# Optimization experiments

Hardware: AMD Instinct MI355X
Metric: run time of the kernel (lower is better)

Reference implementation:

```python
import jax, jax.numpy as jnp
import numpy as np

B, T, D, H = 1, 2048, 1024, 16
HD = D // H
STRIDE = T // 256  # hierarchical global stride (T > 512 branch)


def _mha(q_in, k_in, v_in, Wqkv, bqkv, Wo, bo, nh):
    """torch nn.MultiheadAttention (batch_first, eval/no-dropout), returns (out, head-avg attn)."""
    b, tq, d = q_in.shape
    hd = d // nh
    Wq, Wk, Wv = jnp.split(Wqkv, 3, axis=0)
    bq, bk, bv = jnp.split(bqkv, 3)
    def heads(x, W, bb):
        return (x @ W.T + bb).reshape(b, x.shape[1], nh, hd).transpose(0, 2, 1, 3)
    q = heads(q_in, Wq, bq)
    k = heads(k_in, Wk, bk)
    v = heads(v_in, Wv, bv)
    scores = jnp.einsum('bhtd,bhsd->bhts', q, k) / np.float32(np.sqrt(hd))
    attn = jax.nn.softmax(scores, axis=-1)
    out = jnp.einsum('bhts,bhsd->bhtd', attn, v).transpose(0, 2, 1, 3).reshape(b, tq, d)
    return out @ Wo.T + bo, attn.mean(axis=1)


def _interp_linear(x, size):
    """F.interpolate(mode='linear', align_corners=False) along axis 1. x: [B, Ts, C]."""
    ts = x.shape[1]
    src = (jnp.arange(size, dtype=x.dtype) + 0.5) * (ts / size) - 0.5
    src = jnp.clip(src, 0.0, ts - 1)
    i0 = jnp.floor(src).astype(jnp.int32)
    i1 = jnp.minimum(i0 + 1, ts - 1)
    w = (src - i0.astype(x.dtype))[None, :, None]
    return x[:, i0, :] * (1.0 - w) + x[:, i1, :] * w


def setup_inputs() -> dict:
    rng = jax.random.key(0)
    ks = iter(jax.random.split(rng, 32))
    s = 0.02
    n = lambda shape: jax.random.normal(next(ks), shape, dtype=jnp.float32) * s
    return {
        'query': jax.random.normal(next(ks), (B, T, D), jnp.float32),
        'key': jax.random.normal(next(ks), (B, T, D), jnp.float32),
        'value': jax.random.normal(next(ks), (B, T, D), jnp.float32),
        'strategy_probs': jax.nn.softmax(jax.random.normal(next(ks), (B, 4), jnp.float32), -1),
        'Wqkv_lin': n((3 * D, D)), 'b_lin': jnp.zeros((3 * D,), jnp.float32),
        'Wo_lin': n((D, D)), 'bo_lin': jnp.zeros((D,), jnp.float32),
        'sparsity_pattern': jax.random.normal(next(ks), (H, 1, 1), jnp.float32),
        'Wqkv_loc': n((3 * D, D)), 'b_loc': jnp.zeros((3 * D,), jnp.float32),
        'Wo_loc': n((D, D)), 'bo_loc': jnp.zeros((D,), jnp.float32),
        'Wqkv_glb': n((3 * D, D)), 'b_glb': jnp.zeros((3 * D,), jnp.float32),
        'Wo_glb': n((D, D)), 'bo_glb': jnp.zeros((D,), jnp.float32),
        'Wf': n((D, 2 * D)), 'bf': jnp.zeros((D,), jnp.float32),
        'R_quant': jax.random.normal(next(ks), (H, HD, HD), jnp.float32),
        'ent_gate': jax.random.normal(next(ks), (H, 2, 2), jnp.float32),
    }


def reference(query, key, value, strategy_probs, Wqkv_lin, b_lin, Wo_lin, bo_lin,
              sparsity_pattern, Wqkv_loc, b_loc, Wo_loc, bo_loc,
              Wqkv_glb, b_glb, Wo_glb, bo_glb, Wf, bf, R_quant, ent_gate):
    b, t, d = query.shape
    hd = d // H
    scale = np.float32(np.sqrt(hd))
    # --- 1) "linear" branch: standard MHA ---
    linear_out, linear_w = _mha(query, key, value, Wqkv_lin, b_lin, Wo_lin, bo_lin, H)
    # --- 2) sparse branch (per-head learned on/off mask on raw scores) ---
    qh = query.reshape(b, t, H, hd).transpose(0, 2, 1, 3)
    kh = key.reshape(b, t, H, hd).transpose(0, 2, 1, 3)
    vh = value.reshape(b, t, H, hd).transpose(0, 2, 1, 3)
    scores = jnp.einsum('bhtd,bhsd->bhts', qh, kh) / scale
    mask = (jax.nn.sigmoid(sparsity_pattern) > 0.5).astype(scores.dtype)  # [H,1,1]
    sp_attn = jax.nn.softmax(scores * mask[None], axis=-1)
    sparse_out = jnp.einsum('bhts,bhsd->bhtd', sp_attn, vh).transpose(0, 2, 1, 3).reshape(b, t, d)
    sparse_w = sp_attn.mean(axis=1)
    # --- 3) hierarchical branch (T > 512 path: strided global + linear interp) ---
    local_out, _ = _mha(query, key, value, Wqkv_loc, b_loc, Wo_loc, bo_loc, H // 2)
    gq, gk, gv = query[:, ::STRIDE], key[:, ::STRIDE], value[:, ::STRIDE]
    g_small, _ = _mha(gq, gk, gv, Wqkv_glb, b_glb, Wo_glb, bo_glb, H // 2)
    global_out = _interp_linear(g_small, t)
    hier_out = jnp.concatenate([local_out, global_out], axis=-1) @ Wf.T + bf
    # --- 4) quantum branch (per-head rotation + scalar gate on scores) ---
    q_rot = jnp.einsum('bhtd,hde->bhte', qh, R_quant)
    k_rot = jnp.einsum('bhtd,hde->bhte', kh, R_quant)
    gate = jax.nn.sigmoid(ent_gate[:, 0, 0])[None, :, None, None]  # [1,H,1,1]
    q_attn = jax.nn.softmax((jnp.einsum('bhtd,bhsd->bhts', q_rot, k_rot) / scale) * gate, axis=-1)
    quantum_out = jnp.einsum('bhts,bhsd->bhtd', q_attn, vh).transpose(0, 2, 1, 3).reshape(b, t, d)
    quantum_w = q_attn.mean(axis=1)
    # --- blend via strategy probabilities ---
    sp = strategy_probs[:, :, None]  # [B,4,1]
    all_out = jnp.stack([linear_out, sparse_out, hier_out, quantum_out], axis=1)  # [B,4,T,D]
    weighted = (all_out * sp[..., None]).sum(axis=1)  # [B,T,D]
    wstack = jnp.stack([linear_w, sparse_w, quantum_w], axis=1)  # [B,3,T,T]
    wsel = sp[:, jnp.array([0, 1, 3])][..., None, None]  # [B,3,1,1,1] (faithful to source; requires B==1)
    combined = (wstack * wsel).sum(axis=1)
    return weighted, combined
```

## Files before the change

### kernel.cpp

```cpp
#include <hip/hip_runtime.h>
#include <math.h>

#define D_MODEL 1024

typedef __attribute__((ext_vector_type(8))) short bf16x8;
typedef __attribute__((ext_vector_type(4))) float f32x4;
typedef __attribute__((ext_vector_type(8))) unsigned short u16x8;

__device__ __forceinline__ unsigned short bfr(float f) {
    unsigned u = __float_as_uint(f);
    u += 0x7fffu + ((u >> 16) & 1u);
    return (unsigned short)(u >> 16);
}
__device__ __forceinline__ float bff(unsigned short s) {
    return __uint_as_float(((unsigned)s) << 16);
}
__device__ __forceinline__ void split2(float x, unsigned short &h, unsigned short &l) {
    h = bfr(x);
    l = bfr(x - bff(h));
}
__device__ __forceinline__ f32x4 mfma3(bf16x8 ah, bf16x8 al, bf16x8 bh, bf16x8 bl, f32x4 c) {
    c = __builtin_amdgcn_mfma_f32_16x16x32_bf16(ah, bh, c, 0, 0, 0);
    c = __builtin_amdgcn_mfma_f32_16x16x32_bf16(ah, bl, c, 0, 0, 0);
    c = __builtin_amdgcn_mfma_f32_16x16x32_bf16(al, bh, c, 0, 0, 0);
    return c;
}

__global__ __launch_bounds__(256) void split_rm(
    const float* __restrict__ in, unsigned short* __restrict__ hi,
    unsigned short* __restrict__ lo, int n4)
{
    int idx = blockIdx.x * 256 + threadIdx.x;
    if (idx >= n4) return;
    float4 v = ((const float4*)in)[idx];
    ushort4 hs, ls;
    split2(v.x, hs.x, ls.x); split2(v.y, hs.y, ls.y);
    split2(v.z, hs.z, ls.z); split2(v.w, hs.w, ls.w);
    ((ushort4*)hi)[idx] = hs;
    ((ushort4*)lo)[idx] = ls;
}

__global__ __launch_bounds__(256) void split_tr(
    const float* __restrict__ in, unsigned short* __restrict__ hi,
    unsigned short* __restrict__ lo, int T)
{
    __shared__ float xs[64][65];
    const int t0 = blockIdx.x * 64, d0 = blockIdx.y * 64;
    for (int idx = threadIdx.x; idx < 64 * 16; idx += 256) {
        int r = idx >> 4, c4 = (idx & 15) * 4;
        float4 v = *(const float4*)&in[(size_t)(t0 + r) * D_MODEL + d0 + c4];
        xs[r][c4] = v.x; xs[r][c4 + 1] = v.y; xs[r][c4 + 2] = v.z; xs[r][c4 + 3] = v.w;
    }
    __syncthreads();
    for (int idx = threadIdx.x; idx < 64 * 8; idx += 256) {
        int dd = idx >> 3, t8 = (idx & 7) * 8;
        u16x8 hs, ls;
#pragma unroll
        for (int j = 0; j < 8; ++j) {
            unsigned short hh, ll;
            split2(xs[t8 + j][dd], hh, ll);
            hs[j] = hh; ls[j] = ll;
        }
        *(u16x8*)&hi[(size_t)(d0 + dd) * T + t0 + t8] = hs;
        *(u16x8*)&lo[(size_t)(d0 + dd) * T + t0 + t8] = ls;
    }
}

__global__ __launch_bounds__(256) void gemm_mfma(
    const float* __restrict__ X, int xrstride,
    const float* __restrict__ W, int wrstride,
    const float* __restrict__ bias,
    float* __restrict__ C, int M, int N, int K,
    const float* __restrict__ sptr, int sidx, int accum)
{
    __shared__ unsigned short Xh[64][40], Xl[64][40];
    __shared__ unsigned short Wh[64][40], Wl[64][40];
    const int tid = threadIdx.x;
    const int m0 = blockIdx.x * 64, n0 = blockIdx.y * 64;
    const int lane = tid & 63, wave = tid >> 6;
    const int c = lane & 15, quad = lane >> 4;
    const int mbase = wave * 16;

    f32x4 acc[4];
#pragma unroll
    for (int nt = 0; nt < 4; ++nt) acc[nt] = (f32x4){0.f, 0.f, 0.f, 0.f};

    float4 xr[2], wr[2];
    const int r_ = tid >> 3, d4_ = (tid & 7) * 4;
    const int r2_ = (tid + 256) >> 3, d42_ = ((tid + 256) & 7) * 4;
    auto ldXW = [&](int k0) {
        xr[0] = *(const float4*)&X[(size_t)(m0 + r_) * xrstride + k0 + d4_];
        xr[1] = *(const float4*)&X[(size_t)(m0 + r2_) * xrstride + k0 + d42_];
        wr[0] = *(const float4*)&W[(size_t)(n0 + r_) * wrstride + k0 + d4_];
        wr[1] = *(const float4*)&W[(size_t)(n0 + r2_) * wrstride + k0 + d42_];
    };
    ldXW(0);

    for (int k0 = 0; k0 < K; k0 += 32) {
        __syncthreads();
        {
            ushort4 hs, ls;
            split2(xr[0].x, hs.x, ls.x); split2(xr[0].y, hs.y, ls.y);
            split2(xr[0].z, hs.z, ls.z); split2(xr[0].w, hs.w, ls.w);
            *(ushort4*)&Xh[r_][d4_] = hs; *(ushort4*)&Xl[r_][d4_] = ls;
            split2(xr[1].x, hs.x, ls.x); split2(xr[1].y, hs.y, ls.y);
            split2(xr[1].z, hs.z, ls.z); split2(xr[1].w, hs.w, ls.w);
            *(ushort4*)&Xh[r2_][d42_] = hs; *(ushort4*)&Xl[r2_][d42_] = ls;
            split2(wr[0].x, hs.x, ls.x); split2(wr[0].y, hs.y, ls.y);
            split2(wr[0].z, hs.z, ls.z); split2(wr[0].w, hs.w, ls.w);
            *(ushort4*)&Wh[r_][d4_] = hs; *(ushort4*)&Wl[r_][d4_] = ls;
            split2(wr[1].x, hs.x, ls.x); split2(wr[1].y, hs.y, ls.y);
            split2(wr[1].z, hs.z, ls.z); split2(wr[1].w, hs.w, ls.w);
            *(ushort4*)&Wh[r2_][d42_] = hs; *(ushort4*)&Wl[r2_][d42_] = ls;
        }
        __syncthreads();
        if (k0 + 32 < K) ldXW(k0 + 32);
        bf16x8 ah = *(const bf16x8*)&Xh[mbase + c][quad * 8];
        bf16x8 al = *(const bf16x8*)&Xl[mbase + c][quad * 8];
#pragma unroll
        for (int nt = 0; nt < 4; ++nt) {
            bf16x8 bh = *(const bf16x8*)&Wh[nt * 16 + c][quad * 8];
            bf16x8 bl = *(const bf16x8*)&Wl[nt * 16 + c][quad * 8];
            acc[nt] = mfma3(ah, al, bh, bl, acc[nt]);
        }
    }
    const float s = (sptr != nullptr) ? sptr[sidx] : 1.0f;
#pragma unroll
    for (int nt = 0; nt < 4; ++nt) {
#pragma unroll
        for (int reg = 0; reg < 4; ++reg) {
            int row = m0 + mbase + quad * 4 + reg;
            int col = n0 + nt * 16 + c;
            float v = acc[nt][reg] + (bias ? bias[col] : 0.0f);
            v *= s;
            size_t gi = (size_t)row * N + col;
            if (accum) v += C[gi];
            C[gi] = v;
        }
    }
}

template <int HD>
__global__ __launch_bounds__(256) void flash_mfma(
    const float* __restrict__ Q,
    const unsigned short* __restrict__ Khi, const unsigned short* __restrict__ Klo,
    const unsigned short* __restrict__ Vthi, const unsigned short* __restrict__ Vtlo,
    const float* __restrict__ aparam, int amode,
    float* __restrict__ O, float* __restrict__ O2,
    const float* __restrict__ strat, int o_sidx, int accum,
    float* __restrict__ mout, float* __restrict__ lout,
    int Tq, int Tk, float inv_scale)
{
    constexpr int ROWS = 64;
    constexpr int STILE = (HD == 64) ? 64 : 32;
    constexpr int NT_S = STILE / 16;
    constexpr int KS   = HD / 32;
    constexpr int NT_O = HD / 16;
    constexpr int KS_PV = STILE / 32;
    constexpr int QP = HD + 8;
    constexpr int SP = STILE + 8;
    constexpr int KIT = STILE * HD / 8 / 256;
    constexpr int VIT = STILE * HD / 8 / 256;

    __shared__ __align__(16) unsigned short Kh[STILE][QP], Kl[STILE][QP];
    __shared__ __align__(16) unsigned short Vh[HD][SP],  Vl[HD][SP];
    __shared__ __align__(16) unsigned short Ph[ROWS][SP], Pl[ROWS][SP];

    const int tid = threadIdx.x;
    const int h = blockIdx.y;
    const int r0 = blockIdx.x * ROWS;
    const int lane = tid & 63, wave = tid >> 6;
    const int c = lane & 15, quad = lane >> 4;
    const int mbase = wave * 16;
    const int ZS = gridDim.z;
    const int tkloc = Tk / ZS;
    const int kv0 = blockIdx.z * tkloc;

    float gate = 1.0f;
    if (amode == 1) gate = (aparam[h] > 0.0f) ? 1.0f : 0.0f;
    if (amode == 2) gate = 1.0f / (1.0f + __expf(-aparam[h * 4]));
    const float ascale = gate * inv_scale;
    const bool masked = (amode == 1) && (gate == 0.0f);

    if (masked) {
        for (int idx = tid; idx < ROWS * STILE; idx += 256) {
            int r = idx / STILE, cc = idx % STILE;
            Ph[r][cc] = 0x3F80; Pl[r][cc] = 0;
        }
    }

    bf16x8 qah[KS], qal[KS];
    if (!masked) {
        const float* qrow = &Q[(size_t)(r0 + mbase + c) * D_MODEL + h * HD];
#pragma unroll
        for (int ks = 0; ks < KS; ++ks) {
            float4 a  = *(const float4*)(qrow + ks * 32 + quad * 8);
            float4 b2 = *(const float4*)(qrow + ks * 32 + quad * 8 + 4);
            unsigned short hh, ll;
            split2(a.x, hh, ll);  qah[ks][0] = (short)hh; qal[ks][0] = (short)ll;
            split2(a.y, hh, ll);  qah[ks][1] = (short)hh; qal[ks][1] = (short)ll;
            split2(a.z, hh, ll);  qah[ks][2] = (short)hh; qal[ks][2] = (short)ll;
            split2(a.w, hh, ll);  qah[ks][3] = (short)hh; qal[ks][3] = (short)ll;
            split2(b2.x, hh, ll); qah[ks][4] = (short)hh; qal[ks][4] = (short)ll;
            split2(b2.y, hh, ll); qah[ks][5] = (short)hh; qal[ks][5] = (short)ll;
            split2(b2.z, hh, ll); qah[ks][6] = (short)hh; qal[ks][6] = (short)ll;
            split2(b2.w, hh, ll); qah[ks][7] = (short)hh; qal[ks][7] = (short)ll;
        }
    }

    float mreg[4], lacc[4];
#pragma unroll
    for (int i = 0; i < 4; ++i) { mreg[i] = -1e30f; lacc[i] = 0.0f; }
    f32x4 oacc[NT_O];
#pragma unroll
    for (int nt = 0; nt < NT_O; ++nt) oacc[nt] = (f32x4){0.f, 0.f, 0.f, 0.f};

    u16x8 krh[KIT], krl[KIT], vrh[VIT], vrl[VIT];

    auto load_regs = [&](int s0) {
        if (!masked) {
#pragma unroll
            for (int it = 0; it < KIT; ++it) {
                int idx = tid + it * 256;
                int r = idx / (HD / 8), c8 = (idx % (HD / 8)) * 8;
                size_t go = (size_t)(s0 + r) * D_MODEL + h * HD + c8;
                krh[it] = *(const u16x8*)&Khi[go];
                krl[it] = *(const u16x8*)&Klo[go];
            }
        }
#pragma unroll
        for (int it = 0; it < VIT; ++it) {
            int idx = tid + it * 256;
            int d = idx % HD, s8 = (idx / HD) * 8;
            size_t go = (size_t)(h * HD + d) * Tk + s0 + s8;
            vrh[it] = *(const u16x8*)&Vthi[go];
            vrl[it] = *(const u16x8*)&Vtlo[go];
        }
    };
    auto write_bufs = [&]() {
        if (!masked) {
#pragma unroll
            for (int it = 0; it < KIT; ++it) {
                int idx = tid + it * 256;
                int r = idx / (HD / 8), c8 = (idx % (HD / 8)) * 8;
                *(u16x8*)&Kh[r][c8] = krh[it];
                *(u16x8*)&Kl[r][c8] = krl[it];
            }
        }
#pragma unroll
        for (int it = 0; it < VIT; ++it) {
            int idx = tid + it * 256;
            int d = idx % HD, s8 = (idx / HD) * 8;
            *(u16x8*)&Vh[d][s8] = vrh[it];
            *(u16x8*)&Vl[d][s8] = vrl[it];
        }
    };

    auto compute_tile = [&]() {
        if (!masked) {
            f32x4 sf[NT_S];
#pragma unroll
            for (int nt = 0; nt < NT_S; ++nt) {
                f32x4 s = (f32x4){0.f, 0.f, 0.f, 0.f};
#pragma unroll
                for (int ks = 0; ks < KS; ++ks) {
                    bf16x8 bh = *(const bf16x8*)&Kh[nt * 16 + c][ks * 32 + quad * 8];
                    bf16x8 bl = *(const bf16x8*)&Kl[nt * 16 + c][ks * 32 + quad * 8];
                    s = mfma3(qah[ks], qal[ks], bh, bl, s);
                }
                sf[nt] = s * ascale;
            }
            float tm[4];
#pragma unroll
            for (int reg = 0; reg < 4; ++reg) tm[reg] = sf[0][reg];
#pragma unroll
            for (int nt = 1; nt < NT_S; ++nt)
#pragma unroll
                for (int reg = 0; reg < 4; ++reg) tm[reg] = fmaxf(tm[reg], sf[nt][reg]);
            bool need = (tm[0] > mreg[0] + 8.0f) || (tm[1] > mreg[1] + 8.0f) ||
                        (tm[2] > mreg[2] + 8.0f) || (tm[3] > mreg[3] + 8.0f);
            if (__any(need)) {
#pragma unroll
                for (int off = 1; off < 16; off <<= 1)
#pragma unroll
                    for (int reg = 0; reg < 4; ++reg)
                        tm[reg] = fmaxf(tm[reg], __shfl_xor(tm[reg], off));
#pragma unroll
                for (int reg = 0; reg < 4; ++reg) {
                    float nm = fmaxf(mreg[reg], tm[reg]);
                    float al = __expf(mreg[reg] - nm);
                    mreg[reg] = nm;
                    lacc[reg] *= al;
#pragma unroll
                    for (int nt = 0; nt < NT_O; ++nt) oacc[nt][reg] *= al;
                }
            }
#pragma unroll
            for (int nt = 0; nt < NT_S; ++nt) {
#pragma unroll
                for (int reg = 0; reg < 4; ++reg) {
                    float p = __expf(sf[nt][reg] - mreg[reg]);
                    lacc[reg] += p;
                    unsigned short hh, ll;
                    split2(p, hh, ll);
                    int row = mbase + quad * 4 + reg;
                    Ph[row][nt * 16 + c] = hh;
                    Pl[row][nt * 16 + c] = ll;
                }
            }
        }
        bf16x8 pah[KS_PV], pal[KS_PV];
#pragma unroll
        for (int ks = 0; ks < KS_PV; ++ks) {
            pah[ks] = *(const bf16x8*)&Ph[mbase + c][ks * 32 + quad * 8];
            pal[ks] = *(const bf16x8*)&Pl[mbase + c][ks * 32 + quad * 8];
        }
#pragma unroll
        for (int nt = 0; nt < NT_O; ++nt) {
            f32x4 o = oacc[nt];
#pragma unroll
            for (int ks = 0; ks < KS_PV; ++ks) {
                bf16x8 bh = *(const bf16x8*)&Vh[nt * 16 + c][ks * 32 + quad * 8];
                bf16x8 bl = *(const bf16x8*)&Vl[nt * 16 + c][ks * 32 + quad * 8];
                o = mfma3(pah[ks], pal[ks], bh, bl, o);
            }
            oacc[nt] = o;
        }
    };

    const int NTL = tkloc / STILE;
    load_regs(kv0);
    for (int t = 0; t < NTL; ++t) {
        __syncthreads();
        write_bufs();
        __syncthreads();
        if (t + 1 < NTL) load_regs(kv0 + (t + 1) * STILE);
        compute_tile();
    }

#pragma unroll
    for (int off = 1; off < 16; off <<= 1)
#pragma unroll
        for (int reg = 0; reg < 4; ++reg) lacc[reg] += __shfl_xor(lacc[reg], off);

    if (ZS == 1) {
        const float osc = (o_sidx >= 0) ? strat[o_sidx] : 1.0f;
#pragma unroll
        for (int reg = 0; reg < 4; ++reg) {
            float lf = masked ? (float)Tk : lacc[reg];
            int row = r0 + mbase + quad * 4 + reg;
            if (c == 0) {
                mout[h * Tq + row] = masked ? 0.0f : mreg[reg];
                lout[h * Tq + row] = lf;
            }
            float sc = osc / lf;
#pragma unroll
            for (int nt = 0; nt < NT_O; ++nt) {
                size_t gi = (size_t)row * D_MODEL + h * HD + nt * 16 + c;
                float v = sc * oacc[nt][reg];
                if (accum) v += O[gi];
                O[gi] = v;
            }
        }
    } else {
        float* Op = (blockIdx.z == 0) ? O : O2;
#pragma unroll
        for (int reg = 0; reg < 4; ++reg) {
            float lf = masked ? (float)tkloc : lacc[reg];
            int row = r0 + mbase + quad * 4 + reg;
            if (c == 0) {
                mout[(blockIdx.z * gridDim.y + h) * Tq + row] = masked ? 0.0f : mreg[reg];
                lout[(blockIdx.z * gridDim.y + h) * Tq + row] = lf;
            }
#pragma unroll
            for (int nt = 0; nt < NT_O; ++nt)
                Op[(size_t)row * D_MODEL + h * HD + nt * 16 + c] = oacc[nt][reg];
        }
    }
}

__global__ __launch_bounds__(256) void combine2(
    const float* __restrict__ O0, const float* __restrict__ O1,
    const float* __restrict__ mp, const float* __restrict__ lp,
    float* __restrict__ O, const float* __restrict__ strat,
    int o_sidx, int accum, int Tq)
{
    const int row = blockIdx.x;
    const int c4 = threadIdx.x * 4;
    const int h = c4 >> 7;
    const float m0 = mp[h * Tq + row], m1 = mp[(8 + h) * Tq + row];
    const float l0 = lp[h * Tq + row], l1 = lp[(8 + h) * Tq + row];
    const float m = fmaxf(m0, m1);
    const float w0 = __expf(m0 - m), w1 = __expf(m1 - m);
    const float osc = (o_sidx >= 0) ? strat[o_sidx] : 1.0f;
    const float sc = osc / (l0 * w0 + l1 * w1);
    float4 a = *(const float4*)&O0[(size_t)row * D_MODEL + c4];
    float4 b = *(const float4*)&O1[(size_t)row * D_MODEL + c4];
    size_t gi = (size_t)row * D_MODEL + c4;
    float4 r;
    r.x = sc * (a.x * w0 + b.x * w1);
    r.y = sc * (a.y * w0 + b.y * w1);
    r.z = sc * (a.z * w0 + b.z * w1);
    r.w = sc * (a.w * w0 + b.w * w1);
    if (accum) {
        float4 o = *(const float4*)&O[gi];
        r.x += o.x; r.y += o.y; r.z += o.z; r.w += o.w;
    }
    *(float4*)&O[gi] = r;
}

__global__ __launch_bounds__(256) void comb_mfma(
    const float* __restrict__ Q,
    const unsigned short* __restrict__ Khi, const unsigned short* __restrict__ Klo,
    const float* __restrict__ mrow, const float* __restrict__ lrow,
    const float* __restrict__ aparam, int amode,
    const float* __restrict__ strat,
    float* __restrict__ comb, int Tq, int Tk, int nh, float inv_scale)
{
    __shared__ __align__(16) unsigned short Kh[128][72], Kl[128][72];
    const int tid = threadIdx.x;
    const int r0 = blockIdx.x * 64, c0 = blockIdx.y * 128;
    const int lane = tid & 63, wave = tid >> 6;
    const int c = lane & 15, quad = lane >> 4;
    const int mbase = wave * 16;

    f32x4 acc[8];
#pragma unroll
    for (int nt = 0; nt < 8; ++nt) acc[nt] = (f32x4){0.f, 0.f, 0.f, 0.f};

    int hlist[16]; float glist[16]; int nact = 0; float unif = 0.0f;
    for (int h = 0; h < nh; ++h) {
        float gate = 1.0f;
        if (amode == 1) gate = (aparam[h] > 0.0f) ? 1.0f : 0.0f;
        if (amode == 2) gate = 1.0f / (1.0f + __expf(-aparam[h * 4]));
        if (amode == 1 && gate == 0.0f) { unif += 1.0f; continue; }
        hlist[nact] = h; glist[nact] = gate * inv_scale; ++nact;
    }

    u16x8 krh[4], krl[4];
    auto loadK = [&](int h) {
#pragma unroll
        for (int it = 0; it < 4; ++it) {
            int idx = tid + it * 256;
            int r = idx >> 3, c8 = (idx & 7) * 8;
            size_t go = (size_t)(c0 + r) * D_MODEL + h * 64 + c8;
            krh[it] = *(const u16x8*)&Khi[go];
            krl[it] = *(const u16x8*)&Klo[go];
        }
    };
    if (nact > 0) loadK(hlist[0]);

    for (int i = 0; i < nact; ++i) {
        const int h = hlist[i];
        const float ascale = glist[i];
        __syncthreads();
#pragma unroll
        for (int it = 0; it < 4; ++it) {
            int idx = tid + it * 256;
            int r = idx >> 3, c8 = (idx & 7) * 8;
            *(u16x8*)&Kh[r][c8] = krh[it];
            *(u16x8*)&Kl[r][c8] = krl[it];
        }
        __syncthreads();
        if (i + 1 < nact) loadK(hlist[i + 1]);

        bf16x8 qah[2], qal[2];
        const float* qrow = &Q[(size_t)(r0 + mbase + c) * D_MODEL + h * 64];
#pragma unroll
        for (int ks = 0; ks < 2; ++ks) {
            float4 a  = *(const float4*)(qrow + ks * 32 + quad * 8);
            float4 b2 = *(const float4*)(qrow + ks * 32 + quad * 8 + 4);
            unsigned short hh, ll;
            split2(a.x, hh, ll);  qah[ks][0] = (short)hh; qal[ks][0] = (short)ll;
            split2(a.y, hh, ll);  qah[ks][1] = (short)hh; qal[ks][1] = (short)ll;
            split2(a.z, hh, ll);  qah[ks][2] = (short)hh; qal[ks][2] = (short)ll;
            split2(a.w, hh, ll);  qah[ks][3] = (short)hh; qal[ks][3] = (short)ll;
            split2(b2.x, hh, ll); qah[ks][4] = (short)hh; qal[ks][4] = (short)ll;
            split2(b2.y, hh, ll); qah[ks][5] = (short)hh; qal[ks][5] = (short)ll;
            split2(b2.z, hh, ll); qah[ks][6] = (short)hh; qal[ks][6] = (short)ll;
            split2(b2.w, hh, ll); qah[ks][7] = (short)hh; qal[ks][7] = (short)ll;
        }

        float mr[4], li[4];
#pragma unroll
        for (int reg = 0; reg < 4; ++reg) {
            int row = r0 + mbase + quad * 4 + reg;
            mr[reg] = mrow[h * Tq + row];
            li[reg] = 1.0f / lrow[h * Tq + row];
        }
#pragma unroll
        for (int nt = 0; nt < 8; ++nt) {
            f32x4 s = (f32x4){0.f, 0.f, 0.f, 0.f};
#pragma unroll
            for (int ks = 0; ks < 2; ++ks) {
                bf16x8 bh = *(const bf16x8*)&Kh[nt * 16 + c][ks * 32 + quad * 8];
                bf16x8 bl = *(const bf16x8*)&Kl[nt * 16 + c][ks * 32 + quad * 8];
                s = mfma3(qah[ks], qal[ks], bh, bl, s);
            }
#pragma unroll
            for (int reg = 0; reg < 4; ++reg)
                acc[nt][reg] += __expf(s[reg] * ascale - mr[reg]) * li[reg];
        }
    }
    const float csc = (strat[0] + strat[1] + strat[3]) / (float)nh;
    const float uadd = unif / (float)Tk;
#pragma unroll
    for (int nt = 0; nt < 8; ++nt) {
#pragma unroll
        for (int reg = 0; reg < 4; ++reg) {
            int row = r0 + mbase + quad * 4 + reg;
            comb[(size_t)row * Tk + c0 + nt * 16 + c] = csc * (acc[nt][reg] + uadd);
        }
    }
}

__global__ __launch_bounds__(256) void rotate_heads(
    const float* __restrict__ X, const float* __restrict__ R,
    float* __restrict__ Y)
{
    __shared__ float Rt[64][68];
    __shared__ float xs[64][68];
    const int tid = threadIdx.x;
    const int h = blockIdx.y;
    const int t0 = blockIdx.x * 64;
    for (int idx = tid; idx < 4096; idx += 256) {
        int d = idx >> 6, e = idx & 63;
        Rt[e][d] = R[h * 4096 + idx];
        xs[d][e] = X[(size_t)(t0 + d) * D_MODEL + h * 64 + e];
    }
    __syncthreads();
    const int ty = tid >> 4, tx = tid & 15;
    float acc[4][4] = {};
#pragma unroll 4
    for (int d0 = 0; d0 < 64; d0 += 4) {
        float4 rv[4];
#pragma unroll
        for (int j = 0; j < 4; ++j) rv[j] = *(const float4*)&Rt[tx * 4 + j][d0];
#pragma unroll
        for (int i = 0; i < 4; ++i) {
            float4 a = *(const float4*)&xs[ty * 4 + i][d0];
#pragma unroll
            for (int j = 0; j < 4; ++j)
                acc[i][j] += a.x * rv[j].x + a.y * rv[j].y + a.z * rv[j].z + a.w * rv[j].w;
        }
    }
#pragma unroll
    for (int i = 0; i < 4; ++i)
#pragma unroll
        for (int j = 0; j < 4; ++j)
            Y[(size_t)(t0 + ty * 4 + i) * D_MODEL + h * 64 + tx * 4 + j] = acc[i][j];
}

__global__ __launch_bounds__(256) void interp_lin(
    const float* __restrict__ G, float* __restrict__ out)
{
    const int t = blockIdx.x;
    float src = (t + 0.5f) * 0.125f - 0.5f;
    src = fminf(fmaxf(src, 0.0f), 255.0f);
    float fl = floorf(src);
    int i0 = (int)fl;
    int i1 = min(i0 + 1, 255);
    float w = src - fl;
    const float4* g0 = (const float4*)(G + (size_t)i0 * D_MODEL);
    const float4* g1 = (const float4*)(G + (size_t)i1 * D_MODEL);
    float4* o = (float4*)(out + (size_t)t * D_MODEL);
    int c = threadIdx.x;
    float4 a = g0[c], b = g1[c];
    float4 r;
    r.x = a.x * (1.0f - w) + b.x * w;
    r.y = a.y * (1.0f - w) + b.y * w;
    r.z = a.z * (1.0f - w) + b.z * w;
    r.w = a.w * (1.0f - w) + b.w * w;
    o[c] = r;
}

extern "C" void kernel_launch(void* const* d_in, const int* in_sizes, int n_in,
                              void* d_out, int out_size, void* d_ws, size_t ws_size,
                              hipStream_t stream)
{
    (void)in_sizes; (void)n_in; (void)ws_size; (void)out_size;
    const float* query    = (const float*)d_in[0];
    const float* key      = (const float*)d_in[1];
    const float* value    = (const float*)d_in[2];
    const float* strat    = (const float*)d_in[3];
    const float* Wqkv_lin = (const float*)d_in[4];
    const float* b_lin    = (const float*)d_in[5];
    const float* Wo_lin   = (const float*)d_in[6];
    const float* bo_lin   = (const float*)d_in[7];
    const float* spars    = (const float*)d_in[8];
    const float* Wqkv_loc = (const float*)d_in[9];
    const float* b_loc    = (const float*)d_in[10];
    const float* Wo_loc   = (const float*)d_in[11];
    const float* bo_loc   = (const float*)d_in[12];
    const float* Wqkv_glb = (const float*)d_in[13];
    const float* b_glb    = (const float*)d_in[14];
    const float* Wo_glb   = (const float*)d_in[15];
    const float* bo_glb   = (const float*)d_in[16];
    const float* Wf       = (const float*)d_in[17];
    const float* bf       = (const float*)d_in[18];
    const float* Rq       = (const float*)d_in[19];
    const float* ent      = (const float*)d_in[20];

    float* out = (float*)d_out;
    float* weighted = out;
    float* combined = out + (size_t)2048 * 1024;
    const size_t PLANE = (size_t)2048 * 2048;

    float* ws   = (float*)d_ws;
    float* qkv  = ws;
    float* AO   = qkv + 6291456;
    float* LO   = AO + 2097152;
    float* gqkv = LO + 2097152;
    float* gAO  = gqkv + 786432;
    float* gOUT = gAO + 262144;
    float* GI   = gOUT + 262144;
    float* mb   = GI + 2097152;
    float* lb   = mb + 32768;
    float* qrot = qkv;
    float* krot = qkv + 2097152;
    unsigned short* Ksp_h = (unsigned short*)(lb + 32768);
    unsigned short* Ksp_l = Ksp_h + 2097152;
    unsigned short* Vtp_h = Ksp_l + 2097152;
    unsigned short* Vtp_l = Vtp_h + 2097152;
    unsigned short* gKs_h = Vtp_l + 2097152;
    unsigned short* gKs_l = gKs_h + 262144;
    unsigned short* gVt_h = gKs_l + 262144;
    unsigned short* gVt_l = gVt_h + 262144;

    const float inv8   = 0.125f;
    const float inv128 = 1.0f / sqrtf(128.0f);
    const float* srcs[3] = {query, key, value};

    hipMemsetAsync(weighted, 0, (size_t)2097152 * sizeof(float), stream);

    for (int sl = 0; sl < 3; ++sl)
        gemm_mfma<<<dim3(32, 16), 256, 0, stream>>>(
            srcs[sl], 1024, Wqkv_lin + (size_t)sl * 1048576, 1024, b_lin + sl * 1024,
            qkv + (size_t)sl * 2097152, 2048, 1024, 1024, nullptr, 0, 0);
    split_rm<<<dim3(2048), 256, 0, stream>>>(qkv + 2097152, Ksp_h, Ksp_l, 524288);
    split_tr<<<dim3(32, 16), 256, 0, stream>>>(qkv + 4194304, Vtp_h, Vtp_l, 2048);
    flash_mfma<64><<<dim3(32, 16), 256, 0, stream>>>(
        qkv, Ksp_h, Ksp_l, Vtp_h, Vtp_l, nullptr, 0,
        AO, nullptr, strat, -1, 0, mb, lb, 2048, 2048, inv8);
    comb_mfma<<<dim3(32, 16), 256, 0, stream>>>(
        qkv, Ksp_h, Ksp_l, mb, lb, nullptr, 0, strat,
        combined + 0 * PLANE, 2048, 2048, 16, inv8);
    gemm_mfma<<<dim3(32, 16), 256, 0, stream>>>(
        AO, 1024, Wo_lin, 1024, bo_lin, weighted, 2048, 1024, 1024, strat, 0, 1);

    split_rm<<<dim3(2048), 256, 0, stream>>>(key, Ksp_h, Ksp_l, 524288);
    split_tr<<<dim3(32, 16), 256, 0, stream>>>(value, Vtp_h, Vtp_l, 2048);
    flash_mfma<64><<<dim3(32, 16), 256, 0, stream>>>(
        query, Ksp_h, Ksp_l, Vtp_h, Vtp_l, spars, 1,
        weighted, nullptr, strat, 1, 1, mb, lb, 2048, 2048, inv8);
    comb_mfma<<<dim3(32, 16), 256, 0, stream>>>(
        query, Ksp_h, Ksp_l, mb, lb, spars, 1, strat,
        combined + 1 * PLANE, 2048, 2048, 16, inv8);

    rotate_heads<<<dim3(32, 16), 256, 0, stream>>>(query, Rq, qrot);
    rotate_heads<<<dim3(32, 16), 256, 0, stream>>>(key, Rq, krot);
    split_rm<<<dim3(2048), 256, 0, stream>>>(krot, Ksp_h, Ksp_l, 524288);
    flash_mfma<64><<<dim3(32, 16), 256, 0, stream>>>(
        qrot, Ksp_h, Ksp_l, Vtp_h, Vtp_l, ent, 2,
        weighted, nullptr, strat, 3, 1, mb, lb, 2048, 2048, inv8);
    comb_mfma<<<dim3(32, 16), 256, 0, stream>>>(
        qrot, Ksp_h, Ksp_l, mb, lb, ent, 2, strat,
        combined + 2 * PLANE, 2048, 2048, 16, inv8);

    for (int sl = 0; sl < 3; ++sl)
        gemm_mfma<<<dim3(32, 16), 256, 0, stream>>>(
            srcs[sl], 1024, Wqkv_loc + (size_t)sl * 1048576, 1024, b_loc + sl * 1024,
            qkv + (size_t)sl * 2097152, 2048, 1024, 1024, nullptr, 0, 0);
    split_rm<<<dim3(2048), 256, 0, stream>>>(qkv + 2097152, Ksp_h, Ksp_l, 524288);
    split_tr<<<dim3(32, 16), 256, 0, stream>>>(qkv + 4194304, Vtp_h, Vtp_l, 2048);
    flash_mfma<128><<<dim3(32, 8, 2), 256, 0, stream>>>(
        qkv, Ksp_h, Ksp_l, Vtp_h, Vtp_l, nullptr, 0,
        AO, GI, strat, -1, 0, mb, lb, 2048, 2048, inv128);
    combine2<<<dim3(2048), 256, 0, stream>>>(
        AO, GI, mb, lb, AO, strat, -1, 0, 2048);
    gemm_mfma<<<dim3(32, 16), 256, 0, stream>>>(
        AO, 1024, Wo_loc, 1024, bo_loc, LO, 2048, 1024, 1024, nullptr, 0, 0);

    for (int sl = 0; sl < 3; ++sl)
        gemm_mfma<<<dim3(4, 16), 256, 0, stream>>>(
            srcs[sl], 8192, Wqkv_glb + (size_t)sl * 1048576, 1024, b_glb + sl * 1024,
            gqkv + (size_t)sl * 262144, 256, 1024, 1024, nullptr, 0, 0);
    split_rm<<<dim3(256), 256, 0, stream>>>(gqkv + 262144, gKs_h, gKs_l, 65536);
    split_tr<<<dim3(4, 16), 256, 0, stream>>>(gqkv + 524288, gVt_h, gVt_l, 256);
    flash_mfma<128><<<dim3(4, 8), 256, 0, stream>>>(
        gqkv, gKs_h, gKs_l, gVt_h, gVt_l, nullptr, 0,
        gAO, nullptr, strat, -1, 0, mb, lb, 256, 256, inv128);
    gemm_mfma<<<dim3(4, 16), 256, 0, stream>>>(
        gAO, 1024, Wo_glb, 1024, bo_glb, gOUT, 256, 1024, 1024, nullptr, 0, 0);
    interp_lin<<<dim3(2048), 256, 0, stream>>>(gOUT, GI);

    gemm_mfma<<<dim3(32, 16), 256, 0, stream>>>(
        LO, 1024, Wf, 2048, bf, weighted, 2048, 1024, 1024, strat, 2, 1);
    gemm_mfma<<<dim3(32, 16), 256, 0, stream>>>(
        GI, 1024, Wf + 1024, 2048, nullptr, weighted, 2048, 1024, 1024, strat, 2, 1);
}
```

Measured before the change: 1.291 ms.

## Transpose flash score MFMA to K·Q, pack P with cvt_pk, pre-split Q for comb

The flash kernel now computes the score tile as K×Q so that each lane owns a single query row. That reduces the row max and sum work to one scalar per lane with two cross-lane shuffles, and lets P be written to LDS as packed 64-bit stores built with v_cvt_pk_bf16_f32. The masked path feeds constant one/zero fragments directly instead of filling LDS. comb_mfma now reads Q already split into bf16 hi/lo parts, prepared by new split_rm launches into reused GI scratch, instead of splitting per block. This adds three extra kernel launches and some shuffles when rescaling.

```diff
diff --git a/kernel.cpp b/kernel.cpp
--- a/kernel.cpp
+++ b/kernel.cpp
@@ -18,6 +18,11 @@
 __device__ __forceinline__ void split2(float x, unsigned short &h, unsigned short &l) {
     h = bfr(x);
     l = bfr(x - bff(h));
+}
+__device__ __forceinline__ unsigned cvtpk(float a, float b) {
+    unsigned r;
+    asm("v_cvt_pk_bf16_f32 %0, %1, %2" : "=v"(r) : "v"(a), "v"(b));
+    return r;
 }
 __device__ __forceinline__ f32x4 mfma3(bf16x8 ah, bf16x8 al, bf16x8 bh, bf16x8 bl, f32x4 c) {
     c = __builtin_amdgcn_mfma_f32_16x16x32_bf16(ah, bh, c, 0, 0, 0);
@@ -153,7 +158,7 @@
 {
     constexpr int ROWS = 64;
     constexpr int STILE = (HD == 64) ? 64 : 32;
-    constexpr int NT_S = STILE / 16;
+    constexpr int MT   = STILE / 16;
     constexpr int KS   = HD / 32;
     constexpr int NT_O = HD / 16;
     constexpr int KS_PV = STILE / 32;
@@ -181,13 +186,6 @@
     if (amode == 2) gate = 1.0f / (1.0f + __expf(-aparam[h * 4]));
     const float ascale = gate * inv_scale;
     const bool masked = (amode == 1) && (gate == 0.0f);
-
-    if (masked) {
-        for (int idx = tid; idx < ROWS * STILE; idx += 256) {
-            int r = idx / STILE, cc = idx % STILE;
-            Ph[r][cc] = 0x3F80; Pl[r][cc] = 0;
-        }
-    }
 
     bf16x8 qah[KS], qal[KS];
     if (!masked) {
@@ -208,12 +206,14 @@
         }
     }
 
-    float mreg[4], lacc[4];
-#pragma unroll
-    for (int i = 0; i < 4; ++i) { mreg[i] = -1e30f; lacc[i] = 0.0f; }
+    float mreg = -1e30f, lacc = 0.0f;
     f32x4 oacc[NT_O];
 #pragma unroll
     for (int nt = 0; nt < NT_O; ++nt) oacc[nt] = (f32x4){0.f, 0.f, 0.f, 0.f};
+
+    bf16x8 pone, pzero;
+#pragma unroll
+    for (int j = 0; j < 8; ++j) { pone[j] = (short)0x3F80; pzero[j] = 0; }
 
     u16x8 krh[KIT], krl[KIT], vrh[VIT], vrl[VIT];
 
@@ -258,62 +258,67 @@
 
     auto compute_tile = [&]() {
         if (!masked) {
-            f32x4 sf[NT_S];
-#pragma unroll
-            for (int nt = 0; nt < NT_S; ++nt) {
+            f32x4 sf[MT];
+#pragma unroll
+            for (int mt = 0; mt < MT; ++mt) {
                 f32x4 s = (f32x4){0.f, 0.f, 0.f, 0.f};
 #pragma unroll
                 for (int ks = 0; ks < KS; ++ks) {
-                    bf16x8 bh = *(const bf16x8*)&Kh[nt * 16 + c][ks * 32 + quad * 8];
-                    bf16x8 bl = *(const bf16x8*)&Kl[nt * 16 + c][ks * 32 + quad * 8];
-                    s = mfma3(qah[ks], qal[ks], bh, bl, s);
+                    bf16x8 kh = *(const bf16x8*)&Kh[mt * 16 + c][ks * 32 + quad * 8];
+                    bf16x8 kl = *(const bf16x8*)&Kl[mt * 16 + c][ks * 32 + quad * 8];
+                    s = mfma3(kh, kl, qah[ks], qal[ks], s);
                 }
-                sf[nt] = s * ascale;
-            }
-            float tm[4];
-#pragma unroll
-            for (int reg = 0; reg < 4; ++reg) tm[reg] = sf[0][reg];
-#pragma unroll
-            for (int nt = 1; nt < NT_S; ++nt)
-#pragma unroll
-                for (int reg = 0; reg < 4; ++reg) tm[reg] = fmaxf(tm[reg], sf[nt][reg]);
-            bool need = (tm[0] > mreg[0] + 8.0f) || (tm[1] > mreg[1] + 8.0f) ||
-                        (tm[2] > mreg[2] + 8.0f) || (tm[3] > mreg[3] + 8.0f);
-            if (__any(need)) {
-#pragma unroll
-                for (int off = 1; off < 16; off <<= 1)
-#pragma unroll
-                    for (int reg = 0; reg < 4; ++reg)
-                        tm[reg] = fmaxf(tm[reg], __shfl_xor(tm[reg], off));
-#pragma unroll
-                for (int reg = 0; reg < 4; ++reg) {
-                    float nm = fmaxf(mreg[reg], tm[reg]);
-                    float al = __expf(mreg[reg] - nm);
-                    mreg[reg] = nm;
-                    lacc[reg] *= al;
-#pragma unroll
-                    for (int nt = 0; nt < NT_O; ++nt) oacc[nt][reg] *= al;
-                }
-            }
-#pragma unroll
-            for (int nt = 0; nt < NT_S; ++nt) {
-#pragma unroll
-                for (int reg = 0; reg < 4; ++reg) {
-                    float p = __expf(sf[nt][reg] - mreg[reg]);
-                    lacc[reg] += p;
-                    unsigned short hh, ll;
-                    split2(p, hh, ll);
-                    int row = mbase + quad * 4 + reg;
-                    Ph[row][nt * 16 + c] = hh;
-                    Pl[row][nt * 16 + c] = ll;
-                }
+                sf[mt] = s * ascale;
+            }
+            float tm = sf[0][0];
+#pragma unroll
+            for (int mt = 0; mt < MT; ++mt)
+#pragma unroll
+                for (int reg = 0; reg < 4; ++reg) tm = fmaxf(tm, sf[mt][reg]);
+            if (__any(tm > mreg + 8.0f)) {
+                tm = fmaxf(tm, __shfl_xor(tm, 16));
+                tm = fmaxf(tm, __shfl_xor(tm, 32));
+                float nm = fmaxf(mreg, tm);
+                float al = __expf(mreg - nm);
+                mreg = nm;
+                lacc *= al;
+                float ar[4];
+#pragma unroll
+                for (int reg = 0; reg < 4; ++reg)
+                    ar[reg] = __shfl(al, (lane & 48) | (quad * 4 + reg));
+#pragma unroll
+                for (int nt = 0; nt < NT_O; ++nt)
+#pragma unroll
+                    for (int reg = 0; reg < 4; ++reg) oacc[nt][reg] *= ar[reg];
+            }
+#pragma unroll
+            for (int mt = 0; mt < MT; ++mt) {
+                float p0 = __expf(sf[mt][0] - mreg);
+                float p1 = __expf(sf[mt][1] - mreg);
+                float p2 = __expf(sf[mt][2] - mreg);
+                float p3 = __expf(sf[mt][3] - mreg);
+                lacc += (p0 + p1) + (p2 + p3);
+                unsigned h01 = cvtpk(p0, p1), h23 = cvtpk(p2, p3);
+                float b0 = __uint_as_float(h01 << 16);
+                float b1 = __uint_as_float(h01 & 0xffff0000u);
+                float b2 = __uint_as_float(h23 << 16);
+                float b3 = __uint_as_float(h23 & 0xffff0000u);
+                unsigned l01 = cvtpk(p0 - b0, p1 - b1);
+                unsigned l23 = cvtpk(p2 - b2, p3 - b3);
+                uint2 hw; hw.x = h01; hw.y = h23;
+                uint2 lw; lw.x = l01; lw.y = l23;
+                *(uint2*)&Ph[mbase + c][mt * 16 + quad * 4] = hw;
+                *(uint2*)&Pl[mbase + c][mt * 16 + quad * 4] = lw;
             }
         }
         bf16x8 pah[KS_PV], pal[KS_PV];
 #pragma unroll
         for (int ks = 0; ks < KS_PV; ++ks) {
-            pah[ks] = *(const bf16x8*)&Ph[mbase + c][ks * 32 + quad * 8];
-            pal[ks] = *(const bf16x8*)&Pl[mbase + c][ks * 32 + quad * 8];
+            if (masked) { pah[ks] = pone; pal[ks] = pzero; }
+            else {
+                pah[ks] = *(const bf16x8*)&Ph[mbase + c][ks * 32 + quad * 8];
+                pal[ks] = *(const bf16x8*)&Pl[mbase + c][ks * 32 + quad * 8];
+            }
         }
 #pragma unroll
         for (int nt = 0; nt < NT_O; ++nt) {
@@ -338,40 +343,44 @@
         compute_tile();
     }
 
-#pragma unroll
-    for (int off = 1; off < 16; off <<= 1)
-#pragma unroll
-        for (int reg = 0; reg < 4; ++reg) lacc[reg] += __shfl_xor(lacc[reg], off);
+    lacc += __shfl_xor(lacc, 16);
+    lacc += __shfl_xor(lacc, 32);
 
     if (ZS == 1) {
         const float osc = (o_sidx >= 0) ? strat[o_sidx] : 1.0f;
+        if (quad == 0) {
+            int row = r0 + mbase + c;
+            mout[h * Tq + row] = masked ? 0.0f : mreg;
+            lout[h * Tq + row] = masked ? (float)Tk : lacc;
+        }
+        float sc[4];
 #pragma unroll
         for (int reg = 0; reg < 4; ++reg) {
-            float lf = masked ? (float)Tk : lacc[reg];
+            float lf = masked ? (float)Tk
+                              : __shfl(lacc, (lane & 48) | (quad * 4 + reg));
+            sc[reg] = osc / lf;
+        }
+#pragma unroll
+        for (int reg = 0; reg < 4; ++reg) {
             int row = r0 + mbase + quad * 4 + reg;
-            if (c == 0) {
-                mout[h * Tq + row] = masked ? 0.0f : mreg[reg];
-                lout[h * Tq + row] = lf;
-            }
-            float sc = osc / lf;
 #pragma unroll
             for (int nt = 0; nt < NT_O; ++nt) {
                 size_t gi = (size_t)row * D_MODEL + h * HD + nt * 16 + c;
-                float v = sc * oacc[nt][reg];
+                float v = sc[reg] * oacc[nt][reg];
                 if (accum) v += O[gi];
                 O[gi] = v;
             }
         }
     } else {
         float* Op = (blockIdx.z == 0) ? O : O2;
+        if (quad == 0) {
+            int row = r0 + mbase + c;
+            mout[(blockIdx.z * gridDim.y + h) * Tq + row] = masked ? 0.0f : mreg;
+            lout[(blockIdx.z * gridDim.y + h) * Tq + row] = masked ? (float)tkloc : lacc;
+        }
 #pragma unroll
         for (int reg = 0; reg < 4; ++reg) {
-            float lf = masked ? (float)tkloc : lacc[reg];
             int row = r0 + mbase + quad * 4 + reg;
-            if (c == 0) {
-                mout[(blockIdx.z * gridDim.y + h) * Tq + row] = masked ? 0.0f : mreg[reg];
-                lout[(blockIdx.z * gridDim.y + h) * Tq + row] = lf;
-            }
 #pragma unroll
             for (int nt = 0; nt < NT_O; ++nt)
                 Op[(size_t)row * D_MODEL + h * HD + nt * 16 + c] = oacc[nt][reg];
@@ -410,7 +419,7 @@
 }
 
 __global__ __launch_bounds__(256) void comb_mfma(
-    const float* __restrict__ Q,
+    const unsigned short* __restrict__ Qhi, const unsigned short* __restrict__ Qlo,
     const unsigned short* __restrict__ Khi, const unsigned short* __restrict__ Klo,
     const float* __restrict__ mrow, const float* __restrict__ lrow,
     const float* __restrict__ aparam, int amode,
@@ -465,20 +474,12 @@
         if (i + 1 < nact) loadK(hlist[i + 1]);
 
         bf16x8 qah[2], qal[2];
-        const float* qrow = &Q[(size_t)(r0 + mbase + c) * D_MODEL + h * 64];
+        const unsigned short* qh = &Qhi[(size_t)(r0 + mbase + c) * D_MODEL + h * 64];
+        const unsigned short* ql = &Qlo[(size_t)(r0 + mbase + c) * D_MODEL + h * 64];
 #pragma unroll
         for (int ks = 0; ks < 2; ++ks) {
-            float4 a  = *(const float4*)(qrow + ks * 32 + quad * 8);
-            float4 b2 = *(const float4*)(qrow + ks * 32 + quad * 8 + 4);
-            unsigned short hh, ll;
-            split2(a.x, hh, ll);  qah[ks][0] = (short)hh; qal[ks][0] = (short)ll;
-            split2(a.y, hh, ll);  qah[ks][1] = (short)hh; qal[ks][1] = (short)ll;
-            split2(a.z, hh, ll);  qah[ks][2] = (short)hh; qal[ks][2] = (short)ll;
-            split2(a.w, hh, ll);  qah[ks][3] = (short)hh; qal[ks][3] = (short)ll;
-            split2(b2.x, hh, ll); qah[ks][4] = (short)hh; qal[ks][4] = (short)ll;
-            split2(b2.y, hh, ll); qah[ks][5] = (short)hh; qal[ks][5] = (short)ll;
-            split2(b2.z, hh, ll); qah[ks][6] = (short)hh; qal[ks][6] = (short)ll;
-            split2(b2.w, hh, ll); qah[ks][7] = (short)hh; qal[ks][7] = (short)ll;
+            qah[ks] = *(const bf16x8*)(qh + ks * 32 + quad * 8);
+            qal[ks] = *(const bf16x8*)(ql + ks * 32 + quad * 8);
         }
 
         float mr[4], li[4];
@@ -626,6 +627,8 @@
     unsigned short* gKs_l = gKs_h + 262144;
     unsigned short* gVt_h = gKs_l + 262144;
     unsigned short* gVt_l = gVt_h + 262144;
+    unsigned short* Qsp_h = (unsigned short*)GI;
+    unsigned short* Qsp_l = Qsp_h + 2097152;
 
     const float inv8   = 0.125f;
     const float inv128 = 1.0f / sqrtf(128.0f);
@@ -642,8 +645,9 @@
     flash_mfma<64><<<dim3(32, 16), 256, 0, stream>>>(
         qkv, Ksp_h, Ksp_l, Vtp_h, Vtp_l, nullptr, 0,
         AO, nullptr, strat, -1, 0, mb, lb, 2048, 2048, inv8);
+    split_rm<<<dim3(2048), 256, 0, stream>>>(qkv, Qsp_h, Qsp_l, 524288);
     comb_mfma<<<dim3(32, 16), 256, 0, stream>>>(
-        qkv, Ksp_h, Ksp_l, mb, lb, nullptr, 0, strat,
+        Qsp_h, Qsp_l, Ksp_h, Ksp_l, mb, lb, nullptr, 0, strat,
         combined + 0 * PLANE, 2048, 2048, 16, inv8);
     gemm_mfma<<<dim3(32, 16), 256, 0, stream>>>(
         AO, 1024, Wo_lin, 1024, bo_lin, weighted, 2048, 1024, 1024, strat, 0, 1);
@@ -653,8 +657,9 @@
     flash_mfma<64><<<dim3(32, 16), 256, 0, stream>>>(
         query, Ksp_h, Ksp_l, Vtp_h, Vtp_l, spars, 1,
         weighted, nullptr, strat, 1, 1, mb, lb, 2048, 2048, inv8);
+    split_rm<<<dim3(2048), 256, 0, stream>>>(query, Qsp_h, Qsp_l, 524288);
     comb_mfma<<<dim3(32, 16), 256, 0, stream>>>(
-        query, Ksp_h, Ksp_l, mb, lb, spars, 1, strat,
+        Qsp_h, Qsp_l, Ksp_h, Ksp_l, mb, lb, spars, 1, strat,
         combined + 1 * PLANE, 2048, 2048, 16, inv8);
 
     rotate_heads<<<dim3(32, 16), 256, 0, stream>>>(query, Rq, qrot);
@@ -663,8 +668,9 @@
     flash_mfma<64><<<dim3(32, 16), 256, 0, stream>>>(
         qrot, Ksp_h, Ksp_l, Vtp_h, Vtp_l, ent, 2,
         weighted, nullptr, strat, 3, 1, mb, lb, 2048, 2048, inv8);
+    split_rm<<<dim3(2048), 256, 0, stream>>>(qrot, Qsp_h, Qsp_l, 524288);
     comb_mfma<<<dim3(32, 16), 256, 0, stream>>>(
-        qrot, Ksp_h, Ksp_l, mb, lb, ent, 2, strat,
+        Qsp_h, Qsp_l, Ksp_h, Ksp_l, mb, lb, ent, 2, strat,
         combined + 2 * PLANE, 2048, 2048, 16, inv8);
 
     for (int sl = 0; sl < 3; ++sl)
```

Result: faster. 1.253 ms (-2.9%).
